# Kernel tuning notes

Measured on AMD Instinct MI355X. Metric: run time of the kernel, lower is better.

The kernel has to match this reference:

```python
import jax, jax.numpy as jnp
import numpy as np

RANK = 8
ALPHA = 8.0 / RANK  # module stores alpha/rank


def setup_inputs() -> dict:
    key = jax.random.key(0)
    k1, k2, k3, k4, k5 = jax.random.split(key, 5)
    M, N = 4096, 4096          # out_features, in_features
    T = 8192                   # flattened batch*seq tokens
    x = jax.random.normal(k1, (T, N), dtype=jnp.float32)
    W = jax.random.normal(k2, (M, N), dtype=jnp.float32) * 0.02
    b = jax.random.normal(k3, (M,), dtype=jnp.float32) * 0.02
    A = jax.random.normal(k4, (M, RANK), dtype=jnp.float32) * 0.01
    B = jax.random.normal(k5, (N, RANK), dtype=jnp.float32) * 0.01
    return {"x": x, "W": W, "b": b, "A": A, "B": B}


def reference(x, W, b, A, B):
    # Faithful to the torch module: delta_W = alpha * (A @ B.T) is materialized
    # [M, N], then out = linear(x) + F.linear(x, delta_W).
    delta_W = ALPHA * (A @ B.T)                 # [M, N]
    return x @ W.T + b + x @ delta_W.T          # [T, M]
```

## Files before the change

### kernel.cpp

```cpp
#include <hip/hip_runtime.h>
#include <hip/hip_bf16.h>
#include <cstdint>
#include <cstddef>


#define T_DIM 8192
#define M_DIM 4096
#define N_DIM 4096
#define RANK  8
#define ALPHA 1.0f

typedef _Float16 f16x8 __attribute__((ext_vector_type(8)));
typedef float    f32x4 __attribute__((ext_vector_type(4)));

__global__ void build_weff(const float* __restrict__ W,
                           const float* __restrict__ A,
                           const float* __restrict__ B,
                           _Float16* __restrict__ Weff) {
    int idx = blockIdx.x * blockDim.x + threadIdx.x;
    int m = idx >> 9;
    int n = (idx & 511) << 3;
    float a[RANK];
    const float* Am = A + m * RANK;
#pragma unroll
    for (int r = 0; r < RANK; ++r) a[r] = Am[r];
    const float* Wrow = W + (size_t)m * N_DIM + n;
    f16x8 o;
#pragma unroll
    for (int j = 0; j < 8; ++j) {
        const float* Bn = B + (size_t)(n + j) * RANK;
        float acc = 0.f;
#pragma unroll
        for (int r = 0; r < RANK; ++r) acc += a[r] * Bn[r];
        o[j] = (_Float16)(Wrow[j] + ALPHA * acc);
    }
    *(f16x8*)(Weff + (size_t)m * N_DIM + n) = o;
}

__global__ void cvt_x(const float* __restrict__ x, _Float16* __restrict__ xh) {
    size_t i = ((size_t)blockIdx.x * blockDim.x + threadIdx.x) * 8;
    f32x4 v0 = *(const f32x4*)(x + i);
    f32x4 v1 = *(const f32x4*)(x + i + 4);
    f16x8 o;
    o[0] = (_Float16)v0[0]; o[1] = (_Float16)v0[1];
    o[2] = (_Float16)v0[2]; o[3] = (_Float16)v0[3];
    o[4] = (_Float16)v1[0]; o[5] = (_Float16)v1[1];
    o[6] = (_Float16)v1[2]; o[7] = (_Float16)v1[3];
    *(f16x8*)(xh + i) = o;
}


__device__ static inline void gld_lds16(const void* g, void* l) {
    __builtin_amdgcn_global_load_lds(
        (const __attribute__((address_space(1))) unsigned int*)g,
        (__attribute__((address_space(3))) unsigned int*)l, 16, 0, 0);
}

__global__ __launch_bounds__(256, 2)
void gemm_f16(const _Float16* __restrict__ X, const _Float16* __restrict__ Wt,
              const float* __restrict__ bias, float* __restrict__ out) {
    __shared__ __align__(16) _Float16 lA[128 * 32];
    __shared__ __align__(16) _Float16 lB[128 * 32];

    const int tid  = threadIdx.x;
    const int lane = tid & 63;
    const int wave = tid >> 6;
    const int wr = wave >> 1, wc = wave & 1;
    const int bx = blockIdx.x, by = blockIdx.y;

    const size_t rowX0 = (size_t)by * 128;
    const size_t rowW0 = (size_t)bx * 128;

    const int srow = tid >> 2;
    const int scol = (tid & 3) << 3;

    const int fr = lane & 15;
    const int fk = (lane >> 4) << 3;

    f32x4 acc[4][4] = {};

    for (int k0 = 0; k0 < N_DIM; k0 += 32) {
        gld_lds16(X  + (rowX0      + srow) * N_DIM + k0 + scol, &lA[tid * 8]);
        gld_lds16(X  + (rowX0 + 64 + srow) * N_DIM + k0 + scol, &lA[2048 + tid * 8]);
        gld_lds16(Wt + (rowW0      + srow) * N_DIM + k0 + scol, &lB[tid * 8]);
        gld_lds16(Wt + (rowW0 + 64 + srow) * N_DIM + k0 + scol, &lB[2048 + tid * 8]);
        asm volatile("s_waitcnt vmcnt(0)" ::: "memory");
        __syncthreads();

        f16x8 af[4], bf[4];
#pragma unroll
        for (int i = 0; i < 4; ++i)
            af[i] = *(const f16x8*)&lA[(wr * 64 + i * 16 + fr) * 32 + fk];
#pragma unroll
        for (int i = 0; i < 4; ++i)
            bf[i] = *(const f16x8*)&lB[(wc * 64 + i * 16 + fr) * 32 + fk];
#pragma unroll
        for (int i = 0; i < 4; ++i)
#pragma unroll
            for (int j = 0; j < 4; ++j)
                acc[i][j] = __builtin_amdgcn_mfma_f32_16x16x32_f16(
                    af[i], bf[j], acc[i][j], 0, 0, 0);
        __syncthreads();
    }

    const int crow0 = by * 128 + wr * 64;
    const int ccol0 = bx * 128 + wc * 64;
#pragma unroll
    for (int j = 0; j < 4; ++j) {
        const int col = ccol0 + j * 16 + (lane & 15);
        const float bv = bias[col];
#pragma unroll
        for (int i = 0; i < 4; ++i) {
            const int row = crow0 + i * 16 + ((lane >> 4) << 2);
#pragma unroll
            for (int r = 0; r < 4; ++r)
                out[(size_t)(row + r) * M_DIM + col] = acc[i][j][r] + bv;
        }
    }
}

extern "C" void kernel_launch(void* const* d_in, const int* in_sizes, int n_in,
                              void* d_out, int out_size, void* d_ws, size_t ws_size,
                              hipStream_t stream) {
    const float* x = (const float*)d_in[0];
    const float* W = (const float*)d_in[1];
    const float* b = (const float*)d_in[2];
    const float* A = (const float*)d_in[3];
    const float* B = (const float*)d_in[4];
    float* out = (float*)d_out;

    _Float16* Weff = (_Float16*)d_ws;
    _Float16* Xh   = (_Float16*)((char*)d_ws + (size_t)M_DIM * N_DIM * sizeof(_Float16));

    build_weff<<<(M_DIM / 8) * N_DIM / 256, 256, 0, stream>>>(W, A, B, Weff);
    cvt_x<<<((size_t)T_DIM * N_DIM / 8) / 256, 256, 0, stream>>>(x, Xh);

    dim3 grid(M_DIM / 128, T_DIM / 128);
    gemm_f16<<<grid, dim3(256, 1, 1), 0, stream>>>(Xh, Weff, b, out);
}
```

Before: 651.4 us.

## Apply LoRA term in epilogue via x@B instead of folding into W

```diff
diff --git a/kernel.cpp b/kernel.cpp
--- a/kernel.cpp
+++ b/kernel.cpp
@@ -8,47 +8,74 @@
 #define M_DIM 4096
 #define N_DIM 4096
 #define RANK  8
-#define ALPHA 1.0f
 
 typedef _Float16 f16x8 __attribute__((ext_vector_type(8)));
 typedef float    f32x4 __attribute__((ext_vector_type(4)));
 
-__global__ void build_weff(const float* __restrict__ W,
-                           const float* __restrict__ A,
-                           const float* __restrict__ B,
-                           _Float16* __restrict__ Weff) {
-    int idx = blockIdx.x * blockDim.x + threadIdx.x;
-    int m = idx >> 9;
-    int n = (idx & 511) << 3;
-    float a[RANK];
-    const float* Am = A + m * RANK;
+__global__ __launch_bounds__(256)
+void fuse_x(const float* __restrict__ x, const float* __restrict__ B,
+            _Float16* __restrict__ xh, float* __restrict__ xB) {
+    __shared__ float sred[4][8];
+    const int t   = blockIdx.x;
+    const int tid = threadIdx.x;
+    const int n0  = tid * 16;
+
+    const float* xrow = x + (size_t)t * N_DIM + n0;
+    f32x4 xv[4];
 #pragma unroll
-    for (int r = 0; r < RANK; ++r) a[r] = Am[r];
-    const float* Wrow = W + (size_t)m * N_DIM + n;
+    for (int k = 0; k < 4; ++k) xv[k] = *(const f32x4*)(xrow + k * 4);
+
+    f16x8 h0, h1;
+#pragma unroll
+    for (int k = 0; k < 4; ++k) h0[k] = (_Float16)xv[0][k];
+#pragma unroll
+    for (int k = 0; k < 4; ++k) h0[4 + k] = (_Float16)xv[1][k];
+#pragma unroll
+    for (int k = 0; k < 4; ++k) h1[k] = (_Float16)xv[2][k];
+#pragma unroll
+    for (int k = 0; k < 4; ++k) h1[4 + k] = (_Float16)xv[3][k];
+    *(f16x8*)(xh + (size_t)t * N_DIM + n0)     = h0;
+    *(f16x8*)(xh + (size_t)t * N_DIM + n0 + 8) = h1;
+
+    const float* Bp = B + (size_t)n0 * RANK;
+    f32x4 acc0 = {0.f, 0.f, 0.f, 0.f}, acc1 = {0.f, 0.f, 0.f, 0.f};
+#pragma unroll
+    for (int nn = 0; nn < 16; ++nn) {
+        const float xs = ((const float*)xv)[nn];
+        f32x4 b0 = *(const f32x4*)(Bp + nn * RANK);
+        f32x4 b1 = *(const f32x4*)(Bp + nn * RANK + 4);
+        acc0 += xs * b0;
+        acc1 += xs * b1;
+    }
+
+    float v[8];
+#pragma unroll
+    for (int k = 0; k < 4; ++k) { v[k] = acc0[k]; v[4 + k] = acc1[k]; }
+#pragma unroll
+    for (int off = 32; off > 0; off >>= 1)
+#pragma unroll
+        for (int k = 0; k < 8; ++k) v[k] += __shfl_down(v[k], off);
+    const int lane = tid & 63, wave = tid >> 6;
+    if (lane < 8) sred[wave][lane] = 0.f;
+    if (lane == 0)
+#pragma unroll
+        for (int k = 0; k < 8; ++k) sred[wave][k] = v[k];
+    __syncthreads();
+    if (tid < 8)
+        xB[(size_t)t * RANK + tid] =
+            sred[0][tid] + sred[1][tid] + sred[2][tid] + sred[3][tid];
+}
+
+__global__ __launch_bounds__(256)
+void cvt_f16(const float* __restrict__ src, _Float16* __restrict__ dst) {
+    size_t i = ((size_t)blockIdx.x * blockDim.x + threadIdx.x) * 8;
+    f32x4 v0 = *(const f32x4*)(src + i);
+    f32x4 v1 = *(const f32x4*)(src + i + 4);
     f16x8 o;
 #pragma unroll
-    for (int j = 0; j < 8; ++j) {
-        const float* Bn = B + (size_t)(n + j) * RANK;
-        float acc = 0.f;
-#pragma unroll
-        for (int r = 0; r < RANK; ++r) acc += a[r] * Bn[r];
-        o[j] = (_Float16)(Wrow[j] + ALPHA * acc);
-    }
-    *(f16x8*)(Weff + (size_t)m * N_DIM + n) = o;
+    for (int k = 0; k < 4; ++k) { o[k] = (_Float16)v0[k]; o[4 + k] = (_Float16)v1[k]; }
+    *(f16x8*)(dst + i) = o;
 }
-
-__global__ void cvt_x(const float* __restrict__ x, _Float16* __restrict__ xh) {
-    size_t i = ((size_t)blockIdx.x * blockDim.x + threadIdx.x) * 8;
-    f32x4 v0 = *(const f32x4*)(x + i);
-    f32x4 v1 = *(const f32x4*)(x + i + 4);
-    f16x8 o;
-    o[0] = (_Float16)v0[0]; o[1] = (_Float16)v0[1];
-    o[2] = (_Float16)v0[2]; o[3] = (_Float16)v0[3];
-    o[4] = (_Float16)v1[0]; o[5] = (_Float16)v1[1];
-    o[6] = (_Float16)v1[2]; o[7] = (_Float16)v1[3];
-    *(f16x8*)(xh + i) = o;
-}
-
 
 __device__ static inline void gld_lds16(const void* g, void* l) {
     __builtin_amdgcn_global_load_lds(
@@ -58,7 +85,8 @@
 
 __global__ __launch_bounds__(256, 2)
 void gemm_f16(const _Float16* __restrict__ X, const _Float16* __restrict__ Wt,
-              const float* __restrict__ bias, float* __restrict__ out) {
+              const float* __restrict__ bias, const float* __restrict__ A,
+              const float* __restrict__ xB, float* __restrict__ out) {
     __shared__ __align__(16) _Float16 lA[128 * 32];
     __shared__ __align__(16) _Float16 lB[128 * 32];
 
@@ -73,7 +101,6 @@
 
     const int srow = tid >> 2;
     const int scol = (tid & 3) << 3;
-
     const int fr = lane & 15;
     const int fk = (lane >> 4) << 3;
 
@@ -105,16 +132,33 @@
 
     const int crow0 = by * 128 + wr * 64;
     const int ccol0 = bx * 128 + wc * 64;
+
+    f32x4 Ac0[4], Ac1[4];
+    float bv[4];
+    int   colv[4];
 #pragma unroll
     for (int j = 0; j < 4; ++j) {
         const int col = ccol0 + j * 16 + (lane & 15);
-        const float bv = bias[col];
+        colv[j] = col;
+        bv[j]   = bias[col];
+        Ac0[j]  = *(const f32x4*)(A + (size_t)col * RANK);
+        Ac1[j]  = *(const f32x4*)(A + (size_t)col * RANK + 4);
+    }
 #pragma unroll
-        for (int i = 0; i < 4; ++i) {
-            const int row = crow0 + i * 16 + ((lane >> 4) << 2);
+    for (int i = 0; i < 4; ++i) {
 #pragma unroll
-            for (int r = 0; r < 4; ++r)
-                out[(size_t)(row + r) * M_DIM + col] = acc[i][j][r] + bv;
+        for (int r = 0; r < 4; ++r) {
+            const int row = crow0 + i * 16 + ((lane >> 4) << 2) + r;
+            f32x4 xb0 = *(const f32x4*)(xB + (size_t)row * RANK);
+            f32x4 xb1 = *(const f32x4*)(xB + (size_t)row * RANK + 4);
+#pragma unroll
+            for (int j = 0; j < 4; ++j) {
+                float d = xb0[0] * Ac0[j][0] + xb0[1] * Ac0[j][1]
+                        + xb0[2] * Ac0[j][2] + xb0[3] * Ac0[j][3]
+                        + xb1[0] * Ac1[j][0] + xb1[1] * Ac1[j][1]
+                        + xb1[2] * Ac1[j][2] + xb1[3] * Ac1[j][3];
+                out[(size_t)row * M_DIM + colv[j]] = acc[i][j][r] + bv[j] + d;
+            }
         }
     }
 }
@@ -129,12 +173,14 @@
     const float* B = (const float*)d_in[4];
     float* out = (float*)d_out;
 
-    _Float16* Weff = (_Float16*)d_ws;
-    _Float16* Xh   = (_Float16*)((char*)d_ws + (size_t)M_DIM * N_DIM * sizeof(_Float16));
+    _Float16* Wh = (_Float16*)d_ws;
+    _Float16* Xh = (_Float16*)((char*)d_ws + (size_t)M_DIM * N_DIM * 2);
+    float*    xB = (float*)   ((char*)d_ws + (size_t)M_DIM * N_DIM * 2
+                                           + (size_t)T_DIM * N_DIM * 2);
 
-    build_weff<<<(M_DIM / 8) * N_DIM / 256, 256, 0, stream>>>(W, A, B, Weff);
-    cvt_x<<<((size_t)T_DIM * N_DIM / 8) / 256, 256, 0, stream>>>(x, Xh);
+    fuse_x<<<T_DIM, 256, 0, stream>>>(x, B, Xh, xB);
+    cvt_f16<<<((size_t)M_DIM * N_DIM / 8) / 256, 256, 0, stream>>>(W, Wh);
 
     dim3 grid(M_DIM / 128, T_DIM / 128);
-    gemm_f16<<<grid, dim3(256, 1, 1), 0, stream>>>(Xh, Weff, b, out);
+    gemm_f16<<<grid, dim3(256, 1, 1), 0, stream>>>(Xh, Wh, b, A, xB, out);
 }
```

Result: slower. 702.0 us (+7.8%).
